# Kernel optimization log

Measured on AMD Instinct MI355X. Metric: run time of the kernel, lower is better.

Reference implementation:

```python
import jax, jax.numpy as jnp
import numpy as np


def setup_inputs() -> dict:
    key = jax.random.key(0)
    k1, k2, k3 = jax.random.split(key, 3)
    B, L, D, C = 4, 4096, 1024, 1
    x = jax.random.normal(k1, (B, L, D), dtype=jnp.float32)
    kernel = jax.random.normal(k2, (C, D, L), dtype=jnp.float32)
    Dskip = jax.random.normal(k3, (C, D), dtype=jnp.float32)
    return {"x": x, "kernel": kernel, "D": Dskip}


def reference(x, kernel, D):
    # x: [B, L, H]  kernel: [C, H, L]  D: [C, H]
    L = x.shape[1]
    n = 2 * L
    xt = jnp.transpose(x, (0, 2, 1))  # [B, H, L]
    # soft-threshold the kernel: relu(|k| - 0.1) * sign(k)
    k = jax.nn.relu(jnp.abs(kernel) - 0.1) * jnp.sign(kernel)
    k_f = jnp.fft.rfft(k, n=n)          # [C, H, n//2+1] complex
    x_f = jnp.fft.rfft(xt, n=n)         # [B, H, n//2+1] complex
    y_f = jnp.einsum('bhl,chl->bchl', x_f, k_f)
    y = jnp.fft.irfft(y_f, n=n)[..., :L]            # [B, C, H, L]
    y = y + jnp.einsum('bhl,ch->bchl', xt, D)        # skip term
    # rearrange 'b c h l -> b l (c h)'
    Bn, Cn, Hn, Ln = y.shape
    return jnp.transpose(y, (0, 3, 1, 2)).reshape(Bn, Ln, Cn * Hn)
```

## Files before the change

kernel.cpp:

```cpp
#include <hip/hip_runtime.h>


typedef __attribute__((ext_vector_type(8)))  short s16x8;
typedef __attribute__((ext_vector_type(16))) float f32x16;
typedef __attribute__((ext_vector_type(4)))  float f32x4;
typedef __attribute__((ext_vector_type(4)))  unsigned int u32x4;

constexpr int B_ = 4, L_ = 4096, H_ = 1024;
constexpr int PADX = 256;
constexpr int LX = L_ + PADX;
constexpr int LK = L_ + 32;
constexpr int ST = 256;
constexpr int NST = L_ / ST;

constexpr size_t XT_ELEMS = (size_t)B_ * H_ * LX;
constexpr size_t KR_ELEMS = (size_t)2 * H_ * LK;
constexpr size_t OT_ELEMS = (size_t)B_ * H_ * L_;
constexpr size_t WS_NEEDED = (XT_ELEMS + KR_ELEMS + OT_ELEMS) * sizeof(unsigned short);

constexpr int XS_ROW  = 4320;
constexpr int XS_BLKS = XS_ROW / 8;
constexpr int XS_US   = B_ * XS_ROW;
constexpr int KS_US   = 2 * LK;
constexpr int OAREA_DW = 4 * 132;
constexpr int SMEM_BYTES = XS_US * 2 + KS_US * 2 + 4 * OAREA_DW * 4;

constexpr int nHt = H_ / 64, nLt = L_ / 64;
constexpr int NXB = B_ * nLt * nHt;

__device__ __forceinline__ unsigned short f2bf(float f) {
    unsigned int u = __builtin_bit_cast(unsigned int, f);
    u += 0x7fffu + ((u >> 16) & 1u);
    return (unsigned short)(u >> 16);
}
__device__ __forceinline__ float bf2f(unsigned short u) {
    return __builtin_bit_cast(float, (unsigned int)u << 16);
}

__global__ __launch_bounds__(256)
void prep(const float* __restrict__ x, const float* __restrict__ kin,
          const float* __restrict__ Dk,
          unsigned short* __restrict__ xT, unsigned short* __restrict__ kR)
{
    const int bid = blockIdx.x;
    if (bid < NXB) {
        __shared__ float tile[64][65];
        const int b  = bid / (nLt * nHt);
        const int r0 = bid % (nLt * nHt);
        const int l0 = (r0 / nHt) * 64;
        const int h0 = (r0 % nHt) * 64;
        const int j  = threadIdx.x;
        const int h4 = j & 15;
        const int rg = j >> 4;
        #pragma unroll
        for (int it = 0; it < 4; ++it) {
            const int lr = rg + 16 * it;
            const f32x4 v = *(const f32x4*)(x + ((size_t)b * L_ + l0 + lr) * H_ + h0 + 4 * h4);
            tile[lr][4 * h4 + 0] = v.x; tile[lr][4 * h4 + 1] = v.y;
            tile[lr][4 * h4 + 2] = v.z; tile[lr][4 * h4 + 3] = v.w;
        }
        __syncthreads();
        const int lg = j & 7;
        #pragma unroll
        for (int pp = 0; pp < 2; ++pp) {
            const int hh = (j >> 3) + 32 * pp;
            unsigned int w0 = (unsigned int)f2bf(tile[8*lg+0][hh]) | ((unsigned int)f2bf(tile[8*lg+1][hh]) << 16);
            unsigned int w1 = (unsigned int)f2bf(tile[8*lg+2][hh]) | ((unsigned int)f2bf(tile[8*lg+3][hh]) << 16);
            unsigned int w2 = (unsigned int)f2bf(tile[8*lg+4][hh]) | ((unsigned int)f2bf(tile[8*lg+5][hh]) << 16);
            unsigned int w3 = (unsigned int)f2bf(tile[8*lg+6][hh]) | ((unsigned int)f2bf(tile[8*lg+7][hh]) << 16);
            const u32x4 v = {w0, w1, w2, w3};
            *(u32x4*)(xT + ((size_t)b * H_ + h0 + hh) * LX + PADX + l0 + 8 * lg) = v;
        }
        if (l0 == 0) {
            #pragma unroll
            for (int it = 0; it < 8; ++it) {
                const int idx = j + 256 * it;
                const int row = idx >> 5, off = idx & 31;
                const u32x4 z = {};
                *(u32x4*)(xT + ((size_t)b * H_ + h0 + row) * LX + off * 8) = z;
            }
        }
    } else {
        const int h = bid - NXB;
        const float Dv = Dk[h];
        for (int l = (int)threadIdx.x; l < L_; l += 256) {
            const float a = kin[(size_t)h * L_ + l];
            float v = copysignf(fmaxf(fabsf(a) - 0.1f, 0.0f), a);
            if (l == 0) v += Dv;
            const unsigned short bv = f2bf(v);
            kR[(size_t)h * LK + (L_ - 1 - l)] = bv;
            if (l <= L_ - 2)
                kR[((size_t)H_ + h) * LK + (L_ - 2 - l)] = bv;
        }
        if (threadIdx.x < 32) kR[(size_t)h * LK + L_ + threadIdx.x] = 0;
        if (threadIdx.x < 33) kR[((size_t)H_ + h) * LK + (L_ - 1) + threadIdx.x] = 0;
    }
}

#define BODY(DO0, DO1, DO2, DO3)                                            \
  {                                                                         \
    _Pragma("unroll")                                                       \
    for (int i = 0; i < 16; ++i) {                                          \
      u32x4 aw;                                                             \
      aw.x = abase[8*i+0]; aw.y = abase[8*i+1];                             \
      aw.z = abase[8*i+2]; aw.w = abase[8*i+3];                             \
      const s16x8 af = __builtin_bit_cast(s16x8, aw);                       \
      const int io = 32 * (i >> 1);                                         \
      if (DO3) acc3 = __builtin_amdgcn_mfma_f32_32x32x16_bf16(              \
            af, *(const s16x8*)(((i & 1) ? t3b : t3a) + io), acc3, 0,0,0);  \
      if (DO2) acc2 = __builtin_amdgcn_mfma_f32_32x32x16_bf16(              \
            af, *(const s16x8*)(((i & 1) ? t2b : t2a) + io), acc2, 0,0,0);  \
      if (DO1) acc1 = __builtin_amdgcn_mfma_f32_32x32x16_bf16(              \
            af, *(const s16x8*)(((i & 1) ? t1b : t1a) + io), acc1, 0,0,0);  \
      if (DO0) acc0 = __builtin_amdgcn_mfma_f32_32x32x16_bf16(              \
            af, *(const s16x8*)(((i & 1) ? t0b : t0a) + io), acc0, 0,0,0);  \
    }                                                                       \
    abase -= 128;                                                           \
    if (DO3) { t3a -= 256; t3b -= 256; }                                    \
    if (DO2) { t2a -= 256; t2b -= 256; }                                    \
    if (DO1) { t1a -= 256; t1b -= 256; }                                    \
    if (DO0) { t0a -= 256; t0b -= 256; }                                    \
  }

__global__ __launch_bounds__(256, 2)
void longconv_main(const unsigned short* __restrict__ xT,
                   const unsigned short* __restrict__ kR,
                   unsigned int* __restrict__ outT)
{
    __shared__ __align__(16) unsigned char smem[SMEM_BYTES];
    unsigned short* xs = (unsigned short*)smem;
    unsigned short* ks = (unsigned short*)(smem + (size_t)XS_US * 2);
    float* oarea = (float*)(smem + (size_t)XS_US * 2 + (size_t)KS_US * 2);

    const int h   = blockIdx.x;
    const int tid = threadIdx.x;

    constexpr int NXU = XS_BLKS * 4;
    constexpr int NKU = 2 * (LK / 8);
    for (int u = tid; u < NXU + NKU; u += 256) {
        if (u < NXU) {
            const int b = u / XS_BLKS, n = u - b * XS_BLKS;
            const u32x4 v = *(const u32x4*)(xT + ((size_t)b * H_ + h) * LX + 32 + n * 8);
            *(u32x4*)(xs + (size_t)b * XS_ROW + (size_t)(n ^ b) * 8) = v;
        } else {
            const int v2 = u - NXU;
            const int p = v2 / (LK / 8), i = v2 - p * (LK / 8);
            const u32x4 v = *(const u32x4*)(kR + ((size_t)p * H_ + h) * LK + i * 8);
            *(u32x4*)(ks + (size_t)p * LK + (size_t)i * 8) = v;
        }
    }
    __syncthreads();

    const int w  = tid >> 6, ln = tid & 63;
    const int m  = ln & 31,  q  = ln >> 5;
    const int t  = m >> 2,   b  = m & 3;
    const int si0 = w, si1 = 7 - w, si2 = 8 + w, si3 = 15 - w;

    const int base = 3871 - m + 8 * q;
    const int p    = base & 1;
    const unsigned int* abase = (const unsigned int*)(ks + p * LK + (base - p));
    const unsigned short* xrow = xs + (size_t)b * XS_ROW;
    const int nb = 4 * t + q;

    auto mk = [&](int si, int par) -> const unsigned short* {
        const int n = 32 * si + nb + 2 * par;
        return xrow + (size_t)((n ^ b) * 8);
    };
    const unsigned short *t0a = mk(si0, 0), *t0b = mk(si0, 1);
    const unsigned short *t1a = mk(si1, 0), *t1b = mk(si1, 1);
    const unsigned short *t2a = mk(si2, 0), *t2b = mk(si2, 1);
    const unsigned short *t3a = mk(si3, 0), *t3b = mk(si3, 1);

    f32x16 acc0 = {}, acc1 = {}, acc2 = {}, acc3 = {};
    int beta = 0;
    for (; beta <= si0; ++beta) BODY(1, 1, 1, 1);
    for (; beta <= si1; ++beta) BODY(0, 1, 1, 1);
    for (; beta <= si2; ++beta) BODY(0, 0, 1, 1);
    for (; beta <= si3; ++beta) BODY(0, 0, 0, 1);

    float* ar = oarea + w * OAREA_DW;
    auto writeout = [&](const f32x16& acc, int si) {
        const int Ls = si * ST;
        #pragma unroll
        for (int rh = 0; rh < 2; ++rh) {
            #pragma unroll
            for (int rr2 = 0; rr2 < 2; ++rr2) {
                const int base4 = (8 * rr2 + 4 * q + 4 * t) & 15;
                f32x4 qd;
                qd.x = acc[4 * (2 * rh + rr2) + 0];
                qd.y = acc[4 * (2 * rh + rr2) + 1];
                qd.z = acc[4 * (2 * rh + rr2) + 2];
                qd.w = acc[4 * (2 * rh + rr2) + 3];
                *(f32x4*)(ar + b * 132 + 16 * t + base4) = qd;
            }
            __asm__ volatile("s_waitcnt lgkmcnt(0)" ::: "memory");
            #pragma unroll
            for (int bb = 0; bb < 4; ++bb) {
                const int g  = ln >> 3;
                const int uu = (2 * ln) & 15;
                const int s  = (uu + 4 * g) & 15;
                const float v0 = ar[bb * 132 + 16 * g + s];
                const float v1 = ar[bb * 132 + 16 * g + s + 1];
                const int l = 32 * g + 16 * rh + uu;
                const unsigned int pk =
                    (unsigned int)f2bf(v0) | ((unsigned int)f2bf(v1) << 16);
                outT[(((size_t)bb * H_ + h) * L_ + Ls + l) >> 1] = pk;
            }
            __asm__ volatile("s_waitcnt lgkmcnt(0)" ::: "memory");
        }
    };
    writeout(acc0, si0);
    writeout(acc1, si1);
    writeout(acc2, si2);
    writeout(acc3, si3);
}

__global__ __launch_bounds__(256)
void untranspose(const unsigned short* __restrict__ outT, float* __restrict__ out)
{
    __shared__ float tile[64][65];
    const int bid = blockIdx.x;
    const int b  = bid / (nLt * nHt);
    const int r0 = bid % (nLt * nHt);
    const int l0 = (r0 / nHt) * 64;
    const int h0 = (r0 % nHt) * 64;
    const int j  = threadIdx.x;
    const int lg = j & 7;
    #pragma unroll
    for (int pp = 0; pp < 2; ++pp) {
        const int hh = (j >> 3) + 32 * pp;
        const u32x4 v = *(const u32x4*)(outT + ((size_t)b * H_ + h0 + hh) * L_ + l0 + 8 * lg);
        const unsigned short* pu = (const unsigned short*)&v;
        #pragma unroll
        for (int i = 0; i < 8; ++i) tile[8 * lg + i][hh] = bf2f(pu[i]);
    }
    __syncthreads();
    const int hg = j & 15;
    #pragma unroll
    for (int pp = 0; pp < 4; ++pp) {
        const int ll = (j >> 4) + 16 * pp;
        f32x4 v;
        v.x = tile[ll][4 * hg + 0];
        v.y = tile[ll][4 * hg + 1];
        v.z = tile[ll][4 * hg + 2];
        v.w = tile[ll][4 * hg + 3];
        *(f32x4*)(out + ((size_t)b * L_ + l0 + ll) * H_ + h0 + 4 * hg) = v;
    }
}

constexpr int TLf = 32, Uf = 8, Wf = TLf + Uf - 1, HTf = 256;

__global__ __launch_bounds__(HTf)
void longconv_fp32(const float* __restrict__ x, const float* __restrict__ k,
                   const float* __restrict__ Dskip, float* __restrict__ out)
{
    const int h  = blockIdx.y * HTf + threadIdx.x;
    const int b  = blockIdx.z;
    const int lt = (int)gridDim.x - 1 - (int)blockIdx.x;
    const int L0 = lt * TLf;
    const float* __restrict__ xb = x + ((size_t)b * L_) * H_ + h;
    const float* __restrict__ kh = k + (size_t)h * L_;
    float acc[TLf]; float win[Wf];
    #pragma unroll
    for (int i = 0; i < Wf; ++i) {
        const int idx = L0 - (Uf - 1) + i;
        win[i] = (idx >= 0) ? xb[(size_t)idx * H_] : 0.0f;
    }
    const float Dv = Dskip[h];
    #pragma unroll
    for (int jj = 0; jj < TLf; ++jj) acc[jj] = win[jj + Uf - 1] * Dv;
    const int cmax = L0 / Uf + (TLf / Uf) - 1;
    for (int c = 0; c <= cmax; ++c) {
        float kr[Uf];
        #pragma unroll
        for (int u = 0; u < Uf; ++u) {
            const float a = kh[c * Uf + u];
            kr[u] = copysignf(fmaxf(fabsf(a) - 0.1f, 0.0f), a);
        }
        #pragma unroll
        for (int u = 0; u < Uf; ++u)
            #pragma unroll
            for (int jj = 0; jj < TLf; ++jj)
                acc[jj] = fmaf(kr[u], win[jj + (Uf - 1) - u], acc[jj]);
        if (c < cmax) {
            #pragma unroll
            for (int i = Wf - 1; i >= Uf; --i) win[i] = win[i - Uf];
            #pragma unroll
            for (int i = 0; i < Uf; ++i) {
                const int idx = L0 - (c + 1) * Uf - (Uf - 1) + i;
                win[i] = (idx >= 0) ? xb[(size_t)idx * H_] : 0.0f;
            }
        }
    }
    float* __restrict__ ob = out + ((size_t)b * L_ + L0) * H_ + h;
    #pragma unroll
    for (int jj = 0; jj < TLf; ++jj) ob[(size_t)jj * H_] = acc[jj];
}

extern "C" void kernel_launch(void* const* d_in, const int* in_sizes, int n_in,
                              void* d_out, int out_size, void* d_ws, size_t ws_size,
                              hipStream_t stream)
{
    const float* x  = (const float*)d_in[0];
    const float* k  = (const float*)d_in[1];
    const float* Dk = (const float*)d_in[2];
    float* out = (float*)d_out;

    if (ws_size >= WS_NEEDED) {
        unsigned short* xT = (unsigned short*)d_ws;
        unsigned short* kR = xT + XT_ELEMS;
        unsigned short* oT = kR + KR_ELEMS;
        prep<<<dim3(NXB + H_), dim3(256), 0, stream>>>(x, k, Dk, xT, kR);
        longconv_main<<<dim3(H_), dim3(256), 0, stream>>>(xT, kR, (unsigned int*)oT);
        untranspose<<<dim3(NXB), dim3(256), 0, stream>>>(oT, out);
    } else {
        dim3 grid(L_ / TLf, H_ / HTf, B_);
        longconv_fp32<<<grid, dim3(HTf), 0, stream>>>(x, k, Dk, out);
    }
}
```

Measured before the change: 215.1 us.

## Fuse prep, conv and untranspose into one persistent kernel with grid barriers

Merges the three launches (transpose/convert prep, MFMA Toeplitz conv, untranspose) into one persistent kernel of 512 blocks separated by atomic-counter grid barriers. The kernel soft-threshold and reversal now happen directly into shared memory per head, which drops the kR workspace round trip. The intent is to remove launch gaps and global kernel traffic. In exchange, each block handles two heads in sequence, a memset is added, and correctness depends on all 512 blocks being co-resident, since otherwise the spin barrier deadlocks.

```diff
diff --git a/kernel.cpp b/kernel.cpp
--- a/kernel.cpp
+++ b/kernel.cpp
@@ -11,12 +11,10 @@
 constexpr int LX = L_ + PADX;
 constexpr int LK = L_ + 32;
 constexpr int ST = 256;
-constexpr int NST = L_ / ST;
 
 constexpr size_t XT_ELEMS = (size_t)B_ * H_ * LX;
-constexpr size_t KR_ELEMS = (size_t)2 * H_ * LK;
 constexpr size_t OT_ELEMS = (size_t)B_ * H_ * L_;
-constexpr size_t WS_NEEDED = (XT_ELEMS + KR_ELEMS + OT_ELEMS) * sizeof(unsigned short);
+constexpr size_t WS_NEEDED = (XT_ELEMS + OT_ELEMS) * sizeof(unsigned short) + 64;
 
 constexpr int XS_ROW  = 4320;
 constexpr int XS_BLKS = XS_ROW / 8;
@@ -27,6 +25,7 @@
 
 constexpr int nHt = H_ / 64, nLt = L_ / 64;
 constexpr int NXB = B_ * nLt * nHt;
+constexpr int GRID = 512;
 
 __device__ __forceinline__ unsigned short f2bf(float f) {
     unsigned int u = __builtin_bit_cast(unsigned int, f);
@@ -37,64 +36,17 @@
     return __builtin_bit_cast(float, (unsigned int)u << 16);
 }
 
-__global__ __launch_bounds__(256)
-void prep(const float* __restrict__ x, const float* __restrict__ kin,
-          const float* __restrict__ Dk,
-          unsigned short* __restrict__ xT, unsigned short* __restrict__ kR)
-{
-    const int bid = blockIdx.x;
-    if (bid < NXB) {
-        __shared__ float tile[64][65];
-        const int b  = bid / (nLt * nHt);
-        const int r0 = bid % (nLt * nHt);
-        const int l0 = (r0 / nHt) * 64;
-        const int h0 = (r0 % nHt) * 64;
-        const int j  = threadIdx.x;
-        const int h4 = j & 15;
-        const int rg = j >> 4;
-        #pragma unroll
-        for (int it = 0; it < 4; ++it) {
-            const int lr = rg + 16 * it;
-            const f32x4 v = *(const f32x4*)(x + ((size_t)b * L_ + l0 + lr) * H_ + h0 + 4 * h4);
-            tile[lr][4 * h4 + 0] = v.x; tile[lr][4 * h4 + 1] = v.y;
-            tile[lr][4 * h4 + 2] = v.z; tile[lr][4 * h4 + 3] = v.w;
-        }
-        __syncthreads();
-        const int lg = j & 7;
-        #pragma unroll
-        for (int pp = 0; pp < 2; ++pp) {
-            const int hh = (j >> 3) + 32 * pp;
-            unsigned int w0 = (unsigned int)f2bf(tile[8*lg+0][hh]) | ((unsigned int)f2bf(tile[8*lg+1][hh]) << 16);
-            unsigned int w1 = (unsigned int)f2bf(tile[8*lg+2][hh]) | ((unsigned int)f2bf(tile[8*lg+3][hh]) << 16);
-            unsigned int w2 = (unsigned int)f2bf(tile[8*lg+4][hh]) | ((unsigned int)f2bf(tile[8*lg+5][hh]) << 16);
-            unsigned int w3 = (unsigned int)f2bf(tile[8*lg+6][hh]) | ((unsigned int)f2bf(tile[8*lg+7][hh]) << 16);
-            const u32x4 v = {w0, w1, w2, w3};
-            *(u32x4*)(xT + ((size_t)b * H_ + h0 + hh) * LX + PADX + l0 + 8 * lg) = v;
-        }
-        if (l0 == 0) {
-            #pragma unroll
-            for (int it = 0; it < 8; ++it) {
-                const int idx = j + 256 * it;
-                const int row = idx >> 5, off = idx & 31;
-                const u32x4 z = {};
-                *(u32x4*)(xT + ((size_t)b * H_ + h0 + row) * LX + off * 8) = z;
-            }
-        }
-    } else {
-        const int h = bid - NXB;
-        const float Dv = Dk[h];
-        for (int l = (int)threadIdx.x; l < L_; l += 256) {
-            const float a = kin[(size_t)h * L_ + l];
-            float v = copysignf(fmaxf(fabsf(a) - 0.1f, 0.0f), a);
-            if (l == 0) v += Dv;
-            const unsigned short bv = f2bf(v);
-            kR[(size_t)h * LK + (L_ - 1 - l)] = bv;
-            if (l <= L_ - 2)
-                kR[((size_t)H_ + h) * LK + (L_ - 2 - l)] = bv;
-        }
-        if (threadIdx.x < 32) kR[(size_t)h * LK + L_ + threadIdx.x] = 0;
-        if (threadIdx.x < 33) kR[((size_t)H_ + h) * LK + (L_ - 1) + threadIdx.x] = 0;
-    }
+__device__ __forceinline__ void grid_barrier(unsigned int* cnt, unsigned int target) {
+    __syncthreads();
+    if (threadIdx.x == 0) {
+        __threadfence();
+        __hip_atomic_fetch_add(cnt, 1u, __ATOMIC_ACQ_REL, __HIP_MEMORY_SCOPE_AGENT);
+        while (__hip_atomic_load(cnt, __ATOMIC_ACQUIRE, __HIP_MEMORY_SCOPE_AGENT) < target) {
+            __builtin_amdgcn_s_sleep(8);
+        }
+        __threadfence();
+    }
+    __syncthreads();
 }
 
 #define BODY(DO0, DO1, DO2, DO3)                                            \
@@ -123,128 +75,187 @@
   }
 
 __global__ __launch_bounds__(256, 2)
-void longconv_main(const unsigned short* __restrict__ xT,
-                   const unsigned short* __restrict__ kR,
-                   unsigned int* __restrict__ outT)
+void longconv_fused(const float* __restrict__ x, const float* __restrict__ kin,
+                    const float* __restrict__ Dk,
+                    unsigned short* __restrict__ xT,
+                    unsigned int* __restrict__ outT,
+                    float* __restrict__ out,
+                    unsigned int* __restrict__ cnt)
 {
     __shared__ __align__(16) unsigned char smem[SMEM_BYTES];
-    unsigned short* xs = (unsigned short*)smem;
-    unsigned short* ks = (unsigned short*)(smem + (size_t)XS_US * 2);
-    float* oarea = (float*)(smem + (size_t)XS_US * 2 + (size_t)KS_US * 2);
-
-    const int h   = blockIdx.x;
-    const int tid = threadIdx.x;
-
-    constexpr int NXU = XS_BLKS * 4;
-    constexpr int NKU = 2 * (LK / 8);
-    for (int u = tid; u < NXU + NKU; u += 256) {
-        if (u < NXU) {
-            const int b = u / XS_BLKS, n = u - b * XS_BLKS;
-            const u32x4 v = *(const u32x4*)(xT + ((size_t)b * H_ + h) * LX + 32 + n * 8);
-            *(u32x4*)(xs + (size_t)b * XS_ROW + (size_t)(n ^ b) * 8) = v;
-        } else {
-            const int v2 = u - NXU;
-            const int p = v2 / (LK / 8), i = v2 - p * (LK / 8);
-            const u32x4 v = *(const u32x4*)(kR + ((size_t)p * H_ + h) * LK + i * 8);
-            *(u32x4*)(ks + (size_t)p * LK + (size_t)i * 8) = v;
-        }
-    }
-    __syncthreads();
-
-    const int w  = tid >> 6, ln = tid & 63;
-    const int m  = ln & 31,  q  = ln >> 5;
-    const int t  = m >> 2,   b  = m & 3;
-    const int si0 = w, si1 = 7 - w, si2 = 8 + w, si3 = 15 - w;
-
-    const int base = 3871 - m + 8 * q;
-    const int p    = base & 1;
-    const unsigned int* abase = (const unsigned int*)(ks + p * LK + (base - p));
-    const unsigned short* xrow = xs + (size_t)b * XS_ROW;
-    const int nb = 4 * t + q;
-
-    auto mk = [&](int si, int par) -> const unsigned short* {
-        const int n = 32 * si + nb + 2 * par;
-        return xrow + (size_t)((n ^ b) * 8);
-    };
-    const unsigned short *t0a = mk(si0, 0), *t0b = mk(si0, 1);
-    const unsigned short *t1a = mk(si1, 0), *t1b = mk(si1, 1);
-    const unsigned short *t2a = mk(si2, 0), *t2b = mk(si2, 1);
-    const unsigned short *t3a = mk(si3, 0), *t3b = mk(si3, 1);
-
-    f32x16 acc0 = {}, acc1 = {}, acc2 = {}, acc3 = {};
-    int beta = 0;
-    for (; beta <= si0; ++beta) BODY(1, 1, 1, 1);
-    for (; beta <= si1; ++beta) BODY(0, 1, 1, 1);
-    for (; beta <= si2; ++beta) BODY(0, 0, 1, 1);
-    for (; beta <= si3; ++beta) BODY(0, 0, 0, 1);
-
-    float* ar = oarea + w * OAREA_DW;
-    auto writeout = [&](const f32x16& acc, int si) {
-        const int Ls = si * ST;
+    const int bid = blockIdx.x;
+    const int j   = threadIdx.x;
+
+    {
+        float (*tile)[65] = (float (*)[65])smem;
+        const int h4 = j & 15, rg = j >> 4, lg = j & 7;
         #pragma unroll
-        for (int rh = 0; rh < 2; ++rh) {
-            #pragma unroll
-            for (int rr2 = 0; rr2 < 2; ++rr2) {
-                const int base4 = (8 * rr2 + 4 * q + 4 * t) & 15;
-                f32x4 qd;
-                qd.x = acc[4 * (2 * rh + rr2) + 0];
-                qd.y = acc[4 * (2 * rh + rr2) + 1];
-                qd.z = acc[4 * (2 * rh + rr2) + 2];
-                qd.w = acc[4 * (2 * rh + rr2) + 3];
-                *(f32x4*)(ar + b * 132 + 16 * t + base4) = qd;
-            }
-            __asm__ volatile("s_waitcnt lgkmcnt(0)" ::: "memory");
-            #pragma unroll
-            for (int bb = 0; bb < 4; ++bb) {
-                const int g  = ln >> 3;
-                const int uu = (2 * ln) & 15;
-                const int s  = (uu + 4 * g) & 15;
-                const float v0 = ar[bb * 132 + 16 * g + s];
-                const float v1 = ar[bb * 132 + 16 * g + s + 1];
-                const int l = 32 * g + 16 * rh + uu;
-                const unsigned int pk =
-                    (unsigned int)f2bf(v0) | ((unsigned int)f2bf(v1) << 16);
-                outT[(((size_t)bb * H_ + h) * L_ + Ls + l) >> 1] = pk;
-            }
-            __asm__ volatile("s_waitcnt lgkmcnt(0)" ::: "memory");
-        }
-    };
-    writeout(acc0, si0);
-    writeout(acc1, si1);
-    writeout(acc2, si2);
-    writeout(acc3, si3);
-}
-
-__global__ __launch_bounds__(256)
-void untranspose(const unsigned short* __restrict__ outT, float* __restrict__ out)
-{
-    __shared__ float tile[64][65];
-    const int bid = blockIdx.x;
-    const int b  = bid / (nLt * nHt);
-    const int r0 = bid % (nLt * nHt);
-    const int l0 = (r0 / nHt) * 64;
-    const int h0 = (r0 % nHt) * 64;
-    const int j  = threadIdx.x;
-    const int lg = j & 7;
-    #pragma unroll
-    for (int pp = 0; pp < 2; ++pp) {
-        const int hh = (j >> 3) + 32 * pp;
-        const u32x4 v = *(const u32x4*)(outT + ((size_t)b * H_ + h0 + hh) * L_ + l0 + 8 * lg);
-        const unsigned short* pu = (const unsigned short*)&v;
+        for (int it = 0; it < NXB / GRID; ++it) {
+            const int tI = bid + GRID * it;
+            const int b  = tI / (nLt * nHt);
+            const int r0 = tI % (nLt * nHt);
+            const int l0 = (r0 / nHt) * 64;
+            const int h0 = (r0 % nHt) * 64;
+            __syncthreads();
+            #pragma unroll
+            for (int rr = 0; rr < 4; ++rr) {
+                const int lr = rg + 16 * rr;
+                const f32x4 v = *(const f32x4*)(x + ((size_t)b * L_ + l0 + lr) * H_ + h0 + 4 * h4);
+                tile[lr][4 * h4 + 0] = v.x; tile[lr][4 * h4 + 1] = v.y;
+                tile[lr][4 * h4 + 2] = v.z; tile[lr][4 * h4 + 3] = v.w;
+            }
+            __syncthreads();
+            #pragma unroll
+            for (int pp = 0; pp < 2; ++pp) {
+                const int hh = (j >> 3) + 32 * pp;
+                unsigned int w0 = (unsigned int)f2bf(tile[8*lg+0][hh]) | ((unsigned int)f2bf(tile[8*lg+1][hh]) << 16);
+                unsigned int w1 = (unsigned int)f2bf(tile[8*lg+2][hh]) | ((unsigned int)f2bf(tile[8*lg+3][hh]) << 16);
+                unsigned int w2 = (unsigned int)f2bf(tile[8*lg+4][hh]) | ((unsigned int)f2bf(tile[8*lg+5][hh]) << 16);
+                unsigned int w3 = (unsigned int)f2bf(tile[8*lg+6][hh]) | ((unsigned int)f2bf(tile[8*lg+7][hh]) << 16);
+                const u32x4 v = {w0, w1, w2, w3};
+                *(u32x4*)(xT + ((size_t)b * H_ + h0 + hh) * LX + PADX + l0 + 8 * lg) = v;
+            }
+            if (l0 == 0) {
+                #pragma unroll
+                for (int z = 0; z < 8; ++z) {
+                    const int idx = j + 256 * z;
+                    const int row = idx >> 5, off = idx & 31;
+                    const u32x4 zz = {};
+                    *(u32x4*)(xT + ((size_t)b * H_ + h0 + row) * LX + off * 8) = zz;
+                }
+            }
+        }
+    }
+    grid_barrier(cnt, GRID);
+
+    {
+        unsigned short* xs = (unsigned short*)smem;
+        unsigned short* ks = (unsigned short*)(smem + (size_t)XS_US * 2);
+        float* oarea = (float*)(smem + (size_t)XS_US * 2 + (size_t)KS_US * 2);
+
+        const int w  = j >> 6, ln = j & 63;
+        const int m  = ln & 31,  q  = ln >> 5;
+        const int t  = m >> 2,   b  = m & 3;
+        const int si0 = w, si1 = 7 - w, si2 = 8 + w, si3 = 15 - w;
+        const int nb = 4 * t + q;
+
+        for (int hi = 0; hi < 2; ++hi) {
+            const int h = bid + GRID * hi;
+            __syncthreads();
+            constexpr int NXU = XS_BLKS * 4;
+            for (int u = j; u < NXU; u += 256) {
+                const int bb = u / XS_BLKS, n = u - bb * XS_BLKS;
+                const u32x4 v = *(const u32x4*)(xT + ((size_t)bb * H_ + h) * LX + 32 + n * 8);
+                *(u32x4*)(xs + (size_t)bb * XS_ROW + (size_t)(n ^ bb) * 8) = v;
+            }
+            {
+                const float Dv = Dk[h];
+                #pragma unroll
+                for (int it = 0; it < L_ / 256; ++it) {
+                    const int l = j + 256 * it;
+                    const float a = kin[(size_t)h * L_ + l];
+                    float v = copysignf(fmaxf(fabsf(a) - 0.1f, 0.0f), a);
+                    if (l == 0) v += Dv;
+                    const unsigned short bv = f2bf(v);
+                    ks[L_ - 1 - l] = bv;
+                    if (l <= L_ - 2) ks[LK + (L_ - 2 - l)] = bv;
+                }
+                if (j < 32) ks[L_ + j] = 0;
+                if (j < 33) ks[LK + (L_ - 1) + j] = 0;
+            }
+            __syncthreads();
+
+            const int base = 3871 - m + 8 * q;
+            const int p    = base & 1;
+            const unsigned int* abase = (const unsigned int*)(ks + p * LK + (base - p));
+            const unsigned short* xrow = xs + (size_t)b * XS_ROW;
+            auto mk = [&](int si, int par) -> const unsigned short* {
+                const int n = 32 * si + nb + 2 * par;
+                return xrow + (size_t)((n ^ b) * 8);
+            };
+            const unsigned short *t0a = mk(si0, 0), *t0b = mk(si0, 1);
+            const unsigned short *t1a = mk(si1, 0), *t1b = mk(si1, 1);
+            const unsigned short *t2a = mk(si2, 0), *t2b = mk(si2, 1);
+            const unsigned short *t3a = mk(si3, 0), *t3b = mk(si3, 1);
+
+            f32x16 acc0 = {}, acc1 = {}, acc2 = {}, acc3 = {};
+            int beta = 0;
+            for (; beta <= si0; ++beta) BODY(1, 1, 1, 1);
+            for (; beta <= si1; ++beta) BODY(0, 1, 1, 1);
+            for (; beta <= si2; ++beta) BODY(0, 0, 1, 1);
+            for (; beta <= si3; ++beta) BODY(0, 0, 0, 1);
+
+            float* ar = oarea + w * OAREA_DW;
+            auto writeout = [&](const f32x16& acc, int si) {
+                const int Ls = si * ST;
+                #pragma unroll
+                for (int rh = 0; rh < 2; ++rh) {
+                    #pragma unroll
+                    for (int rr2 = 0; rr2 < 2; ++rr2) {
+                        const int base4 = (8 * rr2 + 4 * q + 4 * t) & 15;
+                        f32x4 qd;
+                        qd.x = acc[4 * (2 * rh + rr2) + 0];
+                        qd.y = acc[4 * (2 * rh + rr2) + 1];
+                        qd.z = acc[4 * (2 * rh + rr2) + 2];
+                        qd.w = acc[4 * (2 * rh + rr2) + 3];
+                        *(f32x4*)(ar + b * 132 + 16 * t + base4) = qd;
+                    }
+                    __asm__ volatile("s_waitcnt lgkmcnt(0)" ::: "memory");
+                    #pragma unroll
+                    for (int bb = 0; bb < 4; ++bb) {
+                        const int g  = ln >> 3;
+                        const int uu = (2 * ln) & 15;
+                        const int s  = (uu + 4 * g) & 15;
+                        const float v0 = ar[bb * 132 + 16 * g + s];
+                        const float v1 = ar[bb * 132 + 16 * g + s + 1];
+                        const int l = 32 * g + 16 * rh + uu;
+                        const unsigned int pk =
+                            (unsigned int)f2bf(v0) | ((unsigned int)f2bf(v1) << 16);
+                        outT[(((size_t)bb * H_ + h) * L_ + Ls + l) >> 1] = pk;
+                    }
+                    __asm__ volatile("s_waitcnt lgkmcnt(0)" ::: "memory");
+                }
+            };
+            writeout(acc0, si0);
+            writeout(acc1, si1);
+            writeout(acc2, si2);
+            writeout(acc3, si3);
+        }
+    }
+    grid_barrier(cnt, 2 * GRID);
+
+    {
+        float (*tile)[65] = (float (*)[65])smem;
+        const unsigned short* oT = (const unsigned short*)outT;
+        const int lg = j & 7, hg = j & 15;
         #pragma unroll
-        for (int i = 0; i < 8; ++i) tile[8 * lg + i][hh] = bf2f(pu[i]);
-    }
-    __syncthreads();
-    const int hg = j & 15;
-    #pragma unroll
-    for (int pp = 0; pp < 4; ++pp) {
-        const int ll = (j >> 4) + 16 * pp;
-        f32x4 v;
-        v.x = tile[ll][4 * hg + 0];
-        v.y = tile[ll][4 * hg + 1];
-        v.z = tile[ll][4 * hg + 2];
-        v.w = tile[ll][4 * hg + 3];
-        *(f32x4*)(out + ((size_t)b * L_ + l0 + ll) * H_ + h0 + 4 * hg) = v;
+        for (int it = 0; it < NXB / GRID; ++it) {
+            const int tI = bid + GRID * it;
+            const int b  = tI / (nLt * nHt);
+            const int r0 = tI % (nLt * nHt);
+            const int l0 = (r0 / nHt) * 64;
+            const int h0 = (r0 % nHt) * 64;
+            __syncthreads();
+            #pragma unroll
+            for (int pp = 0; pp < 2; ++pp) {
+                const int hh = (j >> 3) + 32 * pp;
+                const u32x4 v = *(const u32x4*)(oT + ((size_t)b * H_ + h0 + hh) * L_ + l0 + 8 * lg);
+                const unsigned short* pu = (const unsigned short*)&v;
+                #pragma unroll
+                for (int i = 0; i < 8; ++i) tile[8 * lg + i][hh] = bf2f(pu[i]);
+            }
+            __syncthreads();
+            #pragma unroll
+            for (int pp = 0; pp < 4; ++pp) {
+                const int ll = (j >> 4) + 16 * pp;
+                f32x4 v;
+                v.x = tile[ll][4 * hg + 0];
+                v.y = tile[ll][4 * hg + 1];
+                v.z = tile[ll][4 * hg + 2];
+                v.w = tile[ll][4 * hg + 3];
+                *(f32x4*)(out + ((size_t)b * L_ + l0 + ll) * H_ + h0 + 4 * hg) = v;
+            }
+        }
     }
 }
 
@@ -301,20 +312,20 @@
                               void* d_out, int out_size, void* d_ws, size_t ws_size,
                               hipStream_t stream)
 {
-    const float* x  = (const float*)d_in[0];
-    const float* k  = (const float*)d_in[1];
-    const float* Dk = (const float*)d_in[2];
+    const float* x   = (const float*)d_in[0];
+    const float* kfp = (const float*)d_in[1];
+    const float* Dk  = (const float*)d_in[2];
     float* out = (float*)d_out;
 
     if (ws_size >= WS_NEEDED) {
-        unsigned short* xT = (unsigned short*)d_ws;
-        unsigned short* kR = xT + XT_ELEMS;
-        unsigned short* oT = kR + KR_ELEMS;
-        prep<<<dim3(NXB + H_), dim3(256), 0, stream>>>(x, k, Dk, xT, kR);
-        longconv_main<<<dim3(H_), dim3(256), 0, stream>>>(xT, kR, (unsigned int*)oT);
-        untranspose<<<dim3(NXB), dim3(256), 0, stream>>>(oT, out);
+        unsigned short* xT  = (unsigned short*)d_ws;
+        unsigned int*   oT  = (unsigned int*)(xT + XT_ELEMS);
+        unsigned int*   cnt = (unsigned int*)(xT + XT_ELEMS + OT_ELEMS);
+        hipMemsetAsync((void*)cnt, 0, 64, stream);
+        longconv_fused<<<dim3(GRID), dim3(256), 0, stream>>>(
+            x, kfp, Dk, xT, oT, out, cnt);
     } else {
         dim3 grid(L_ / TLf, H_ / HTf, B_);
-        longconv_fp32<<<grid, dim3(HTf), 0, stream>>>(x, k, Dk, out);
-    }
-}
+        longconv_fp32<<<grid, dim3(HTf), 0, stream>>>(x, kfp, Dk, out);
+    }
+}
```

New measurement: 373.3 us. +73.6%, slower.
